# Performance work log

Measured on AMD Instinct MI355X. Metric: run time of the kernel, lower is better.

## Reference

```python
import jax, jax.numpy as jnp
import numpy as np

N = 50000      # nodes
E = 800000     # edges (avg degree 16)
DIN = 128
H = 128
DOUT = 64


def setup_inputs() -> dict:
    key = jax.random.key(0)
    ks = jax.random.split(key, 8)
    x = jax.random.normal(ks[0], (N, DIN), dtype=jnp.float32)
    edge_index = jax.random.randint(ks[1], (2, E), 0, N, dtype=jnp.int32)
    def glorot(k, fi, fo):
        return jax.random.normal(k, (fi, fo), dtype=jnp.float32) * (1.0 / np.sqrt(fi))
    return {
        "x": x,
        "edge_index": edge_index,
        "W1": glorot(ks[2], DIN, H), "b1": jnp.zeros((H,), jnp.float32),
        "W2": glorot(ks[3], H, H),   "b2": jnp.zeros((H,), jnp.float32),
        "W3": glorot(ks[4], H, DOUT),"b3": jnp.zeros((DOUT,), jnp.float32),
    }


def reference(x, edge_index, W1, b1, W2, b2, W3, b3):
    n = x.shape[0]
    # GCNConv: add self-loops, symmetric degree normalization D^-1/2 (A+I) D^-1/2
    loop = jnp.arange(n, dtype=edge_index.dtype)
    src = jnp.concatenate([edge_index[0], loop])  # [E+N]
    dst = jnp.concatenate([edge_index[1], loop])
    deg = jax.ops.segment_sum(jnp.ones(src.shape, x.dtype), dst, num_segments=n)
    dinv = jnp.where(deg > 0, jax.lax.rsqrt(deg), 0.0)
    norm = dinv[src] * dinv[dst]  # [E+N]

    def conv(h, W, b):
        h = h @ W                                   # [N, out]
        msg = h[src] * norm[:, None]                # gather + scale
        return jax.ops.segment_sum(msg, dst, num_segments=n) + b

    # gelu after every layer except the last (forward breaks before act)
    h = jax.nn.gelu(conv(x, W1, b1), approximate=False)
    h = jax.nn.gelu(conv(h, W2, b2), approximate=False)
    return conv(h, W3, b3)
```

## Files before the change

### kernel.cpp

```cpp
#include <hip/hip_runtime.h>
#include <math.h>

#define NDIN 128
#define NHID 128
#define NDOUT 64

typedef _Float16 half2_t __attribute__((ext_vector_type(2)));
typedef _Float16 half4_t __attribute__((ext_vector_type(4)));
typedef _Float16 half8_t __attribute__((ext_vector_type(8)));
typedef float    float4v __attribute__((ext_vector_type(4)));

__device__ __forceinline__ float gelu_exact(float x) {
    return 0.5f * x * (1.0f + erff(x * 0.70710678118654752f));
}


__device__ void wtrans_tile(const float* __restrict__ W, _Float16* __restrict__ Wt,
                            int K, int N, int bx, int by) {
    __shared__ float tile[32][33];
    int tx = threadIdx.x & 31, ty = threadIdx.x >> 5;
    for (int i = 0; i < 32; i += 8) {
        int k = by * 32 + ty + i, nn = bx * 32 + tx;
        tile[ty + i][tx] = (k < K && nn < N) ? W[(size_t)k * N + nn] : 0.f;
    }
    __syncthreads();
    for (int i = 0; i < 32; i += 8) {
        int nn = bx * 32 + ty + i, k = by * 32 + tx;
        if (nn < N && k < K) Wt[(size_t)nn * K + k] = (_Float16)tile[tx][ty + i];
    }
}

__global__ __launch_bounds__(256) void prep0_kernel(
    const float* __restrict__ W1, _Float16* __restrict__ W1t,
    const float* __restrict__ W2, _Float16* __restrict__ W2t,
    const float* __restrict__ W3, _Float16* __restrict__ W3t,
    int* __restrict__ count, int* __restrict__ done, int n) {
    int b = blockIdx.x;
    if (b < 16) {
        wtrans_tile(W1, W1t, NDIN, NHID, b & 3, b >> 2);
    } else if (b < 32) {
        wtrans_tile(W2, W2t, NHID, NHID, (b - 16) & 3, (b - 16) >> 2);
    } else if (b < 40) {
        wtrans_tile(W3, W3t, NHID, NDOUT, (b - 32) & 1, (b - 32) >> 1);
    } else {
        int z = b - 40;
        int i = z * 256 + threadIdx.x;
        if (i < n) count[i] = 0;
        if (z == 0 && threadIdx.x == 0) *done = 0;
    }
}


__global__ void count_kernel(const int* __restrict__ dst, int* __restrict__ count, int E) {
    int e = blockIdx.x * blockDim.x + threadIdx.x;
    if (e < E) atomicAdd(&count[dst[e]], 1);
}


__global__ __launch_bounds__(256) void reduce_scanp_kernel(
    const int* __restrict__ count, int* __restrict__ blocksum, int* __restrict__ blockoff,
    int* __restrict__ rowptr, int* __restrict__ done, int nb, int n) {
    __shared__ int s[256];
    __shared__ int islast;
    int t = threadIdx.x;
    int i = blockIdx.x * 256 + t;
    s[t] = (i < n) ? count[i] : 0;
    __syncthreads();
    for (int off = 128; off > 0; off >>= 1) {
        if (t < off) s[t] += s[t + off];
        __syncthreads();
    }
    if (t == 0) {
        atomicExch(&blocksum[blockIdx.x], s[0]);
        __threadfence();
        int old = atomicAdd(done, 1);
        islast = (old == nb - 1) ? 1 : 0;
    }
    __syncthreads();
    if (!islast) return;
    __threadfence();
    int v = (t < nb) ? atomicAdd(&blocksum[t], 0) : 0;
    s[t] = v;
    __syncthreads();
    for (int off = 1; off < 256; off <<= 1) {
        int u = (t >= off) ? s[t - off] : 0;
        __syncthreads();
        s[t] += u;
        __syncthreads();
    }
    if (t < nb) blockoff[t] = s[t] - v;
    if (t == 255) rowptr[n] = s[255];
}


__global__ __launch_bounds__(256) void scan_blocks_kernel(
    const int* __restrict__ count, const int* __restrict__ blockoff,
    int* __restrict__ rowptr, float* __restrict__ dinv, int n) {
    __shared__ int s[256];
    int i = blockIdx.x * 256 + threadIdx.x;
    int v = (i < n) ? count[i] : 0;
    s[threadIdx.x] = v;
    __syncthreads();
    for (int off = 1; off < 256; off <<= 1) {
        int u = (threadIdx.x >= off) ? s[threadIdx.x - off] : 0;
        __syncthreads();
        s[threadIdx.x] += u;
        __syncthreads();
    }
    if (i < n) {
        rowptr[i] = blockoff[blockIdx.x] + s[threadIdx.x] - v;
        dinv[i] = rsqrtf((float)(v + 1));
    }
}


__global__ void fill_kernel(const int* __restrict__ src, const int* __restrict__ dst,
                            const float* __restrict__ dinv, const int* __restrict__ rowptr,
                            int* __restrict__ count, int2* __restrict__ adj, int E) {
    int e = blockIdx.x * blockDim.x + threadIdx.x;
    if (e >= E) return;
    int s = src[e], d = dst[e];
    int slot = atomicSub(&count[d], 1) - 1;
    int p = rowptr[d] + slot;
    adj[p] = make_int2(s, __float_as_int(dinv[s] * dinv[d]));
}


template <int BN, bool AF16>
__global__ __launch_bounds__(256) void gemm_mfma(
    const void* __restrict__ Aptr, const _Float16* __restrict__ Bt,
    _Float16* __restrict__ T, int M) {
    __shared__ _Float16 lds_a[64][136];
    __shared__ _Float16 lds_bt[BN][136];
    const int K = 128;
    int tid = threadIdx.x;
    int bm = blockIdx.x * 64;
    int wave = tid >> 6, lane = tid & 63;
    int m = lane & 15, quad = lane >> 4;

    if (AF16) {
        const _Float16* A = (const _Float16*)Aptr;
#pragma unroll
        for (int j = 0; j < 4; j++) {
            int c = tid + j * 256;
            int r = c >> 4, col = (c & 15) << 3;
            int grow = bm + r;
            uint4 v = make_uint4(0, 0, 0, 0);
            if (grow < M) v = *(const uint4*)(A + (size_t)grow * K + col);
            *(uint4*)&lds_a[r][col] = v;
        }
    } else {
        const float* A = (const float*)Aptr;
#pragma unroll
        for (int j = 0; j < 8; j++) {
            int c = tid + j * 256;
            int r = c >> 5, col = (c & 31) << 2;
            int grow = bm + r;
            float4 v = make_float4(0.f, 0.f, 0.f, 0.f);
            if (grow < M) v = *(const float4*)(A + (size_t)grow * K + col);
            half4_t h;
            h[0] = (_Float16)v.x; h[1] = (_Float16)v.y;
            h[2] = (_Float16)v.z; h[3] = (_Float16)v.w;
            *(half4_t*)&lds_a[r][col] = h;
        }
    }
    {
        const int chunks = BN * K / 8;
        for (int c = tid; c < chunks; c += 256) {
            int r = c >> 4, col = (c & 15) << 3;
            *(uint4*)&lds_bt[r][col] = *(const uint4*)(Bt + (size_t)r * K + col);
        }
    }
    __syncthreads();

    const int NT = BN / 16;
    float4v acc[NT];
#pragma unroll
    for (int nt = 0; nt < NT; nt++) acc[nt] = (float4v){0.f, 0.f, 0.f, 0.f};

    int arow = (wave << 4) + m;
#pragma unroll
    for (int kc = 0; kc < K; kc += 32) {
        half8_t a = *(const half8_t*)&lds_a[arow][kc + quad * 8];
#pragma unroll
        for (int nt = 0; nt < NT; nt++) {
            half8_t b = *(const half8_t*)&lds_bt[nt * 16 + m][kc + quad * 8];
            acc[nt] = __builtin_amdgcn_mfma_f32_16x16x32_f16(a, b, acc[nt], 0, 0, 0);
        }
    }
#pragma unroll
    for (int nt = 0; nt < NT; nt++) {
#pragma unroll
        for (int r = 0; r < 4; r++) {
            int grow = bm + (wave << 4) + (quad << 2) + r;
            if (grow < M) T[(size_t)grow * BN + nt * 16 + m] = (_Float16)acc[nt][r];
        }
    }
}


template <int F, bool DOGELU, bool OUTF16>
__global__ __launch_bounds__(256) void agg_kernel(
    const _Float16* __restrict__ t, const int* __restrict__ rowptr,
    const int2* __restrict__ adj, const float* __restrict__ dinv,
    const float* __restrict__ bias, void* __restrict__ outp, int n) {
    constexpr int LPG = F / 8;
    constexpr int NG  = 64 / LPG;
    int node = (int)((blockIdx.x * blockDim.x + threadIdx.x) >> 6);
    int lane = threadIdx.x & 63;
    if (node >= n) return;

    int g = lane / LPG;
    int lsub = lane % LPG;

    float acc[8];
#pragma unroll
    for (int f = 0; f < 8; f++) acc[f] = 0.f;

    float wself = dinv[node];
    wself *= wself;
    if (g == 0) {
        half8_t u = *(const half8_t*)(t + (size_t)node * F + lsub * 8);
#pragma unroll
        for (int f = 0; f < 8; f++) acc[f] = wself * (float)u[f];
    }

    int beg = rowptr[node];
    int end = rowptr[node + 1];
    for (int e0 = beg; e0 < end; e0 += 64) {
        int rem = end - e0;
        int j = 0; float w = 0.f;
        if (lane < rem) {
            int2 ed = adj[e0 + lane];
            j = ed.x; w = __int_as_float(ed.y);
        }
        int cnt = rem < 64 ? rem : 64;
        int iters = (cnt + NG - 1) / NG;
#pragma unroll 4
        for (int it = 0; it < iters; it++) {
            int srcl = it * NG + g;
            int jj = __shfl(j, srcl);
            float ww = __shfl(w, srcl);
            half8_t u = *(const half8_t*)(t + (size_t)jj * F + lsub * 8);
#pragma unroll
            for (int f = 0; f < 8; f++) acc[f] += ww * (float)u[f];
        }
    }
#pragma unroll
    for (int off = LPG; off < 64; off <<= 1)
#pragma unroll
        for (int f = 0; f < 8; f++) acc[f] += __shfl_xor(acc[f], off);

    if (g == 0) {
        float4 b0 = *(const float4*)(bias + lsub * 8);
        float4 b1 = *(const float4*)(bias + lsub * 8 + 4);
        acc[0] += b0.x; acc[1] += b0.y; acc[2] += b0.z; acc[3] += b0.w;
        acc[4] += b1.x; acc[5] += b1.y; acc[6] += b1.z; acc[7] += b1.w;
        if (DOGELU) {
#pragma unroll
            for (int f = 0; f < 8; f++) acc[f] = gelu_exact(acc[f]);
        }
        if (OUTF16) {
            half8_t o;
#pragma unroll
            for (int f = 0; f < 8; f++) o[f] = (_Float16)acc[f];
            *(half8_t*)((_Float16*)outp + (size_t)node * F + lsub * 8) = o;
        } else {
            float* op = (float*)outp + (size_t)node * F + lsub * 8;
            float4 o0 = make_float4(acc[0], acc[1], acc[2], acc[3]);
            float4 o1 = make_float4(acc[4], acc[5], acc[6], acc[7]);
            *(float4*)op = o0;
            *(float4*)(op + 4) = o1;
        }
    }
}


extern "C" void kernel_launch(void* const* d_in, const int* in_sizes, int n_in,
                              void* d_out, int out_size, void* d_ws, size_t ws_size,
                              hipStream_t stream) {
    const float* x  = (const float*)d_in[0];
    const int* edge = (const int*)d_in[1];
    const float* W1 = (const float*)d_in[2];
    const float* b1 = (const float*)d_in[3];
    const float* W2 = (const float*)d_in[4];
    const float* b2 = (const float*)d_in[5];
    const float* W3 = (const float*)d_in[6];
    const float* b3 = (const float*)d_in[7];
    float* out = (float*)d_out;

    const int N = in_sizes[0] / NDIN;
    const int E = in_sizes[1] / 2;
    const int* src = edge;
    const int* dst = edge + E;
    const int NB = (N + 255) / 256;

    char* p = (char*)d_ws;
    auto alloc = [&](size_t bytes) {
        char* q = p;
        p += (bytes + 255) & ~(size_t)255;
        return q;
    };
    int*       count    = (int*)alloc((size_t)N * 4);
    int*       rowptr   = (int*)alloc((size_t)(N + 1) * 4);
    int*       blocksum = (int*)alloc((size_t)NB * 4);
    int*       blockoff = (int*)alloc((size_t)NB * 4);
    int*       done     = (int*)alloc(256);
    float*     dinv     = (float*)alloc((size_t)N * 4);
    int2*      adj      = (int2*)alloc((size_t)E * 8);
    _Float16*  W1t      = (_Float16*)alloc((size_t)NHID * NDIN * 2);
    _Float16*  W2t      = (_Float16*)alloc((size_t)NHID * NHID * 2);
    _Float16*  W3t      = (_Float16*)alloc((size_t)NDOUT * NHID * 2);
    _Float16*  tbuf     = (_Float16*)alloc((size_t)N * NHID * 2);
    _Float16*  hbuf     = (_Float16*)alloc((size_t)N * NHID * 2);

    dim3 blk(256);
    int mtiles = (N + 63) / 64;
    int eblocks = (E + 255) / 256;
    int agg_blocks = (N + 3) / 4;

    prep0_kernel<<<40 + NB, blk, 0, stream>>>(W1, W1t, W2, W2t, W3, W3t, count, done, N);
    count_kernel<<<eblocks, blk, 0, stream>>>(dst, count, E);
    reduce_scanp_kernel<<<NB, blk, 0, stream>>>(count, blocksum, blockoff, rowptr,
                                                done, NB, N);
    scan_blocks_kernel<<<NB, blk, 0, stream>>>(count, blockoff, rowptr, dinv, N);
    fill_kernel<<<eblocks, blk, 0, stream>>>(src, dst, dinv, rowptr, count, adj, E);
    gemm_mfma<128, false><<<mtiles, blk, 0, stream>>>(x, W1t, tbuf, N);
    agg_kernel<128, true, true><<<agg_blocks, blk, 0, stream>>>(tbuf, rowptr, adj,
                                                                dinv, b1, hbuf, N);
    gemm_mfma<128, true><<<mtiles, blk, 0, stream>>>(hbuf, W2t, tbuf, N);
    agg_kernel<128, true, true><<<agg_blocks, blk, 0, stream>>>(tbuf, rowptr, adj,
                                                                dinv, b2, hbuf, N);
    gemm_mfma<64, true><<<mtiles, blk, 0, stream>>>(hbuf, W3t, tbuf, N);
    agg_kernel<64, false, false><<<agg_blocks, blk, 0, stream>>>(tbuf, rowptr, adj,
                                                                 dinv, b3, out, N);
}
```

Before: 312.1 us.

## Split aggregation feature dimension into 32-wide slices across blocks

Each aggregation block now handles one 32-feature slice (4 lanes × 8 halves) of 4 nodes, so a wave processes 16 edges per iteration instead of 4 (F=128) or 8 (F=64). Block count grows by the slice factor. The aim is more edge-level parallelism per wave, fewer serial iterations for low-degree nodes, and higher occupancy. In exchange the adjacency list, rowptr and dinv are reread once per slice, and each gather fetches only 64 bytes per row, which may hurt memory coalescing.

```diff
diff --git a/kernel.cpp b/kernel.cpp
--- a/kernel.cpp
+++ b/kernel.cpp
@@ -199,19 +199,20 @@
 }
 
 
-template <int F, bool DOGELU, bool OUTF16>
+template <int F, int NSLICE, bool DOGELU, bool OUTF16>
 __global__ __launch_bounds__(256) void agg_kernel(
     const _Float16* __restrict__ t, const int* __restrict__ rowptr,
     const int2* __restrict__ adj, const float* __restrict__ dinv,
     const float* __restrict__ bias, void* __restrict__ outp, int n) {
-    constexpr int LPG = F / 8;
-    constexpr int NG  = 64 / LPG;
-    int node = (int)((blockIdx.x * blockDim.x + threadIdx.x) >> 6);
+    constexpr int SF = F / NSLICE;
+    int slice = blockIdx.x % NSLICE;
+    int node = (blockIdx.x / NSLICE) * 4 + (threadIdx.x >> 6);
     int lane = threadIdx.x & 63;
     if (node >= n) return;
 
-    int g = lane / LPG;
-    int lsub = lane % LPG;
+    int g = lane >> 2;
+    int lsub = lane & 3;
+    int foff = slice * SF + lsub * 8;
 
     float acc[8];
 #pragma unroll
@@ -220,7 +221,7 @@
     float wself = dinv[node];
     wself *= wself;
     if (g == 0) {
-        half8_t u = *(const half8_t*)(t + (size_t)node * F + lsub * 8);
+        half8_t u = *(const half8_t*)(t + (size_t)node * F + foff);
 #pragma unroll
         for (int f = 0; f < 8; f++) acc[f] = wself * (float)u[f];
     }
@@ -235,25 +236,25 @@
             j = ed.x; w = __int_as_float(ed.y);
         }
         int cnt = rem < 64 ? rem : 64;
-        int iters = (cnt + NG - 1) / NG;
+        int iters = (cnt + 15) >> 4;
 #pragma unroll 4
         for (int it = 0; it < iters; it++) {
-            int srcl = it * NG + g;
+            int srcl = (it << 4) + g;
             int jj = __shfl(j, srcl);
             float ww = __shfl(w, srcl);
-            half8_t u = *(const half8_t*)(t + (size_t)jj * F + lsub * 8);
+            half8_t u = *(const half8_t*)(t + (size_t)jj * F + foff);
 #pragma unroll
             for (int f = 0; f < 8; f++) acc[f] += ww * (float)u[f];
         }
     }
 #pragma unroll
-    for (int off = LPG; off < 64; off <<= 1)
+    for (int off = 4; off < 64; off <<= 1)
 #pragma unroll
         for (int f = 0; f < 8; f++) acc[f] += __shfl_xor(acc[f], off);
 
     if (g == 0) {
-        float4 b0 = *(const float4*)(bias + lsub * 8);
-        float4 b1 = *(const float4*)(bias + lsub * 8 + 4);
+        float4 b0 = *(const float4*)(bias + foff);
+        float4 b1 = *(const float4*)(bias + foff + 4);
         acc[0] += b0.x; acc[1] += b0.y; acc[2] += b0.z; acc[3] += b0.w;
         acc[4] += b1.x; acc[5] += b1.y; acc[6] += b1.z; acc[7] += b1.w;
         if (DOGELU) {
@@ -264,13 +265,11 @@
             half8_t o;
 #pragma unroll
             for (int f = 0; f < 8; f++) o[f] = (_Float16)acc[f];
-            *(half8_t*)((_Float16*)outp + (size_t)node * F + lsub * 8) = o;
+            *(half8_t*)((_Float16*)outp + (size_t)node * F + foff) = o;
         } else {
-            float* op = (float*)outp + (size_t)node * F + lsub * 8;
-            float4 o0 = make_float4(acc[0], acc[1], acc[2], acc[3]);
-            float4 o1 = make_float4(acc[4], acc[5], acc[6], acc[7]);
-            *(float4*)op = o0;
-            *(float4*)(op + 4) = o1;
+            float* op = (float*)outp + (size_t)node * F + foff;
+            *(float4*)op = make_float4(acc[0], acc[1], acc[2], acc[3]);
+            *(float4*)(op + 4) = make_float4(acc[4], acc[5], acc[6], acc[7]);
         }
     }
 }
@@ -317,7 +316,9 @@
     dim3 blk(256);
     int mtiles = (N + 63) / 64;
     int eblocks = (E + 255) / 256;
-    int agg_blocks = (N + 3) / 4;
+    int ngroups = (N + 3) / 4;
+    int agg128_blocks = ngroups * 4;
+    int agg64_blocks  = ngroups * 2;
 
     prep0_kernel<<<40 + NB, blk, 0, stream>>>(W1, W1t, W2, W2t, W3, W3t, count, done, N);
     count_kernel<<<eblocks, blk, 0, stream>>>(dst, count, E);
@@ -326,12 +327,12 @@
     scan_blocks_kernel<<<NB, blk, 0, stream>>>(count, blockoff, rowptr, dinv, N);
     fill_kernel<<<eblocks, blk, 0, stream>>>(src, dst, dinv, rowptr, count, adj, E);
     gemm_mfma<128, false><<<mtiles, blk, 0, stream>>>(x, W1t, tbuf, N);
-    agg_kernel<128, true, true><<<agg_blocks, blk, 0, stream>>>(tbuf, rowptr, adj,
-                                                                dinv, b1, hbuf, N);
+    agg_kernel<128, 4, true, true><<<agg128_blocks, blk, 0, stream>>>(
+        tbuf, rowptr, adj, dinv, b1, hbuf, N);
     gemm_mfma<128, true><<<mtiles, blk, 0, stream>>>(hbuf, W2t, tbuf, N);
-    agg_kernel<128, true, true><<<agg_blocks, blk, 0, stream>>>(tbuf, rowptr, adj,
-                                                                dinv, b2, hbuf, N);
+    agg_kernel<128, 4, true, true><<<agg128_blocks, blk, 0, stream>>>(
+        tbuf, rowptr, adj, dinv, b2, hbuf, N);
     gemm_mfma<64, true><<<mtiles, blk, 0, stream>>>(hbuf, W3t, tbuf, N);
-    agg_kernel<64, false, false><<<agg_blocks, blk, 0, stream>>>(tbuf, rowptr, adj,
-                                                                 dinv, b3, out, N);
-}
+    agg_kernel<64, 2, false, false><<<agg64_blocks, blk, 0, stream>>>(
+        tbuf, rowptr, adj, dinv, b3, out, N);
+}
```

After: 428.4 us. 1.37x slower.
